# Kernel tuning notes

Measured on AMD Instinct MI355X. Metric: run time of the kernel, lower is better.

Reference implementation:

```python
import jax, jax.numpy as jnp
import numpy as np

D_MODEL, D_FF, N_EXPERTS, TOP_K = 1024, 2048, 8, 2
B, S = 2, 2048

def setup_inputs() -> dict:
    key = jax.random.key(0)
    k1, k2, k3, k4 = jax.random.split(key, 4)
    scale = 0.02
    return {
        "x": jax.random.normal(k1, (B, S, D_MODEL), dtype=jnp.float32),
        "gate_w": jax.random.normal(k2, (D_MODEL, N_EXPERTS), dtype=jnp.float32) * scale,
        "w1": jax.random.normal(k3, (N_EXPERTS, D_MODEL, D_FF), dtype=jnp.float32) * scale,
        "w2": jax.random.normal(k4, (N_EXPERTS, D_FF, D_MODEL), dtype=jnp.float32) * scale,
    }

def reference(x, gate_w, w1, w2):
    # --- Router (eval mode: no exploration noise, no dropout) ---
    router_logits = jnp.einsum('bsd,de->bse', x, gate_w)          # [B,S,E]
    top_logits, top_idx = jax.lax.top_k(router_logits, TOP_K)      # [B,S,K]
    top_w = jax.nn.softmax(top_logits, axis=-1)                    # [B,S,K]
    # topk indices are distinct per token, so per-(token,expert) combine weight
    # is the sum over k of weight_k * 1[idx_k == e] (matches torch gather/argmax logic)
    combine = jnp.sum(
        jax.nn.one_hot(top_idx, N_EXPERTS, dtype=x.dtype) * top_w[..., None],
        axis=-2)                                                   # [B,S,E]
    # --- Experts: dense-compute formulation of the gather/MLP/scatter loop ---
    h = jax.nn.silu(jnp.einsum('bsd,edf->ebsf', x, w1))            # [E,B,S,Dff]
    y = jnp.einsum('ebsf,efd->ebsd', h, w2)                        # [E,B,S,D]
    out = jnp.einsum('ebsd,bse->bsd', y, combine)                  # [B,S,D]
    return out
```

## Files before the change

kernel.cpp:

```cpp
#include <hip/hip_runtime.h>
#include <cstdint>
#include <cstddef>

#define D_MODEL 1024
#define D_FF    2048
#define N_EXP   8
#define NTOK    4096
#define NASSIGN (NTOK * 2)
#define MAXTILE 72

typedef __bf16 bf16_t;
typedef bf16_t bf16x8 __attribute__((ext_vector_type(8)));
typedef float  f32x4  __attribute__((ext_vector_type(4)));

typedef __attribute__((address_space(3))) void       lds_void;
typedef const __attribute__((address_space(1))) void gl_void;

__device__ __forceinline__ unsigned short f2b(float f) {
  union { float f; unsigned u; } v; v.f = f;
  unsigned u = v.u;
  unsigned r = (u + 0x7FFFu + ((u >> 16) & 1u)) >> 16;
  return (unsigned short)r;
}
__device__ __forceinline__ float b2f(unsigned short b) {
  union { unsigned u; float f; } v; v.u = ((unsigned)b) << 16; return v.f;
}

__device__ __forceinline__ void transpose_tile_128x64(
    const float* __restrict__ ein, unsigned short* __restrict__ eout,
    int R , int C ,
    int r0, int c0, unsigned* T, int tid)
{
  const int g = tid >> 4;
  const int m = tid & 15;

  float4 v[8];
  #pragma unroll
  for (int i = 0; i < 8; ++i)
    v[i] = *(const float4*)(ein + (size_t)(r0 + i * 16 + g) * C + c0 + m * 4);

  #pragma unroll
  for (int i = 0; i < 8; ++i) {
    int r  = i * 16 + g;
    int cx = (r >> 5) << 3;
    unsigned lo = (unsigned)f2b(v[i].x) | ((unsigned)f2b(v[i].y) << 16);
    unsigned hi = (unsigned)f2b(v[i].z) | ((unsigned)f2b(v[i].w) << 16);
    T[r * 33 + ((2 * m)     ^ cx)] = lo;
    T[r * 33 + ((2 * m + 1) ^ cx)] = hi;
  }
  __syncthreads();

  const int c    = tid >> 2;
  const int s4   = tid & 3;
  const int half = (c & 1) * 16;
  const int ccol = (c >> 1) ^ (s4 << 3);
  unsigned ow[16];
  #pragma unroll
  for (int j2 = 0; j2 < 16; ++j2) {
    int r = s4 * 32 + 2 * j2;
    unsigned lo16 = (T[r * 33 + ccol] >> half) & 0xFFFFu;
    unsigned hi16 = (T[(r + 1) * 33 + ccol] >> half) & 0xFFFFu;
    ow[j2] = lo16 | (hi16 << 16);
  }
  uint4* dst = (uint4*)(eout + (size_t)(c0 + c) * R + r0 + s4 * 32);
  dst[0] = *(uint4*)&ow[0];
  dst[1] = *(uint4*)&ow[4];
  dst[2] = *(uint4*)&ow[8];
  dst[3] = *(uint4*)&ow[12];
}

__global__ __launch_bounds__(256) void prep_k(
    const float* __restrict__ x, const float* __restrict__ gw,
    const float* __restrict__ w1, const float* __restrict__ w2,
    unsigned short* __restrict__ w1t, unsigned short* __restrict__ w2t,
    int* __restrict__ eidx, float* __restrict__ ewt)
{
  __shared__ unsigned T[128 * 33];
  const int bid = blockIdx.x;
  const int tid = threadIdx.x;

  if (bid < 2048) {
    int e = bid >> 8, rem = bid & 255;
    int by = rem >> 5, bx = rem & 31;
    transpose_tile_128x64(w1 + (size_t)e * D_MODEL * D_FF,
                          w1t + (size_t)e * D_MODEL * D_FF,
                          D_MODEL, D_FF, by * 128, bx * 64, T, tid);
    return;
  }
  if (bid < 4096) {
    int b = bid - 2048;
    int e = b >> 8, rem = b & 255;
    int by = rem >> 4, bx = rem & 15;
    transpose_tile_128x64(w2 + (size_t)e * D_MODEL * D_FF,
                          w2t + (size_t)e * D_MODEL * D_FF,
                          D_FF, D_MODEL, by * 128, bx * 64, T, tid);
    return;
  }
  const int rb = bid - 4096;
  const int wv = tid >> 6, lane = tid & 63;
  const int token = rb * 4 + wv;
  const float4* xr4 = (const float4*)(x + (size_t)token * D_MODEL);
  const float4* gw4 = (const float4*)gw;

  float acc[8] = {};
  #pragma unroll
  for (int it = 0; it < 4; ++it) {
    float4 xv = xr4[it * 64 + lane];
    int d0 = it * 256 + lane * 4;
    #pragma unroll
    for (int i = 0; i < 4; ++i) {
      int d = d0 + i;
      float4 g0 = gw4[d * 2];
      float4 g1 = gw4[d * 2 + 1];
      float xs = (i == 0) ? xv.x : (i == 1) ? xv.y : (i == 2) ? xv.z : xv.w;
      acc[0] += xs * g0.x; acc[1] += xs * g0.y;
      acc[2] += xs * g0.z; acc[3] += xs * g0.w;
      acc[4] += xs * g1.x; acc[5] += xs * g1.y;
      acc[6] += xs * g1.z; acc[7] += xs * g1.w;
    }
  }
  #pragma unroll
  for (int m = 1; m < 64; m <<= 1) {
    #pragma unroll
    for (int k = 0; k < 8; ++k) acc[k] += __shfl_xor(acc[k], m);
  }
  if (lane == 0) {
    int i1 = 0; float v1 = acc[0];
    #pragma unroll
    for (int k = 1; k < 8; ++k) if (acc[k] > v1) { v1 = acc[k]; i1 = k; }
    int i2 = -1; float v2 = -1e30f;
    #pragma unroll
    for (int k = 0; k < 8; ++k) if (k != i1 && acc[k] > v2) { v2 = acc[k]; i2 = k; }
    float t  = __expf(v2 - v1);
    float wa = 1.f / (1.f + t);
    float wb = t * wa;
    eidx[token * 2 + 0] = i1; eidx[token * 2 + 1] = i2;
    ewt [token * 2 + 0] = wa; ewt [token * 2 + 1] = wb;
  }
}

__global__ __launch_bounds__(1024) void scan_k(
    const int* __restrict__ eidx, const float* __restrict__ ewt,
    int* __restrict__ counts, int* __restrict__ offsets,
    int* __restrict__ rowtok, float* __restrict__ rowwt, int* __restrict__ rowof,
    int* __restrict__ tile_e, int* __restrict__ tile_m0, int* __restrict__ tile_n)
{
  __shared__ int wtot[16][9];
  __shared__ int woff[16][9];
  __shared__ int soff[8];
  const int t = threadIdx.x, w = t >> 6, lane = t & 63;

  int4 a = ((const int4*)eidx)[t * 2];
  int4 b = ((const int4*)eidx)[t * 2 + 1];
  int my[8] = {a.x, a.y, a.z, a.w, b.x, b.y, b.z, b.w};
  int pre[8], local[8] = {};
  #pragma unroll
  for (int i = 0; i < 8; ++i) { pre[i] = local[my[i]]; local[my[i]]++; }

  int inc[8];
  #pragma unroll
  for (int e = 0; e < 8; ++e) inc[e] = local[e];
  #pragma unroll
  for (int d = 1; d < 64; d <<= 1) {
    #pragma unroll
    for (int e = 0; e < 8; ++e) {
      int v = __shfl_up(inc[e], d);
      if (lane >= d) inc[e] += v;
    }
  }
  if (lane == 63) {
    #pragma unroll
    for (int e = 0; e < 8; ++e) wtot[w][e] = inc[e];
  }
  __syncthreads();

  if (t < 8) {
    int e = t, run = 0;
    #pragma unroll
    for (int ww = 0; ww < 16; ++ww) { woff[ww][e] = run; run += wtot[ww][e]; }
    wtot[0][e] = run;
  }
  __syncthreads();

  if (t == 0) {
    int o = 0, tt = 0;
    for (int e = 0; e < 8; ++e) {
      int c = wtot[0][e];
      counts[e] = c;
      offsets[e] = o;
      soff[e] = o;
      int nt = (c + 255) >> 8;
      for (int i = 0; i < nt; ++i) { tile_e[tt] = e; tile_m0[tt] = i * 256; ++tt; }
      o += c;
    }
    tile_n[0] = tt;
  }
  __syncthreads();

  int base_[8];
  #pragma unroll
  for (int e = 0; e < 8; ++e) base_[e] = soff[e] + woff[w][e] + inc[e] - local[e];

  float4 wa4 = ((const float4*)ewt)[t * 2];
  float4 wb4 = ((const float4*)ewt)[t * 2 + 1];
  float wv[8] = {wa4.x, wa4.y, wa4.z, wa4.w, wb4.x, wb4.y, wb4.z, wb4.w};

  #pragma unroll
  for (int i = 0; i < 8; ++i) {
    int bb = t * 8 + i, e = my[i];
    int row = base_[e] + pre[i];
    rowtok[row] = bb >> 1;
    rowwt[row]  = wv[i];
    rowof[bb]   = row;
  }
}

__global__ __launch_bounds__(256) void gather_k(
    const float* __restrict__ x, const int* __restrict__ rowtok,
    unsigned short* __restrict__ Xe)
{
  const int row = blockIdx.x;
  const int token = rowtok[row];
  const float4* xr = (const float4*)(x + (size_t)token * D_MODEL);
  ushort4* dst = (ushort4*)(Xe + (size_t)row * D_MODEL);
  float4 v = xr[threadIdx.x];
  ushort4 o;
  o.x = f2b(v.x); o.y = f2b(v.y); o.z = f2b(v.z); o.w = f2b(v.w);
  dst[threadIdx.x] = o;
}

template<int K, int N, int MODE>
__global__ __launch_bounds__(512) void moe_gemm_k(
    const unsigned short* __restrict__ A,
    const unsigned short* __restrict__ Bt,
    unsigned short* __restrict__ Hout,
    const int* __restrict__ counts, const int* __restrict__ offsets,
    const float* __restrict__ rowwt,
    const int* __restrict__ tile_e, const int* __restrict__ tile_m0,
    const int* __restrict__ tile_n)
{
  constexpr int BN    = 256;
  constexpr int RT    = 512;
  constexpr int LOADS = 8;
  constexpr int JF    = 4;
  constexpr int NT    = K / 64;
  constexpr int NTN   = N / BN;
  constexpr int WN    = 64;

  __shared__ char lds[2 * RT * 128];

  const int nwg = gridDim.x;
  const int bid = blockIdx.x;
  const int wg  = (bid & 7) * (nwg >> 3) + (bid >> 3);
  const int t_  = wg / NTN;
  if (t_ >= tile_n[0]) return;
  const int e    = tile_e[t_];
  const int m0   = tile_m0[t_];
  const int n0   = (wg % NTN) * BN;
  const int cnt  = counts[e];
  const int base = offsets[e];

  const int tid  = threadIdx.x;
  const int l    = tid & 63;
  const int w    = tid >> 6;
  const int wm   = w >> 2;
  const int wn   = w & 3;
  const int col  = l & 15, quad = l >> 4;

  const unsigned short* Aseg = A + (size_t)base * K;
  const unsigned short* Bseg = Bt + (size_t)e * ((size_t)N * K);

  const int w8 = w * 8, l3 = l >> 3;
  const int ckst = ((l & 7) ^ l3) << 3;

  auto stage_one = [&](int n, int k0s, char* bw) {
    const unsigned short* src = (n < 4)
      ? Aseg + (size_t)(m0 + n * 64 + w8 + l3) * K + (k0s + ckst)
      : Bseg + (size_t)(n0 + (n - 4) * 64 + w8 + l3) * K + (k0s + ckst);
    __builtin_amdgcn_global_load_lds((gl_void*)src,
        (lds_void*)(bw + (n * 8 + w) * 1024), 16, 0, 0);
  };

  #pragma unroll
  for (int n = 0; n < LOADS; ++n) stage_one(n, 0, lds);

  const int abyte = (wm * 128 + col) * 128;
  const int bbyte = (256 + wn * WN + col) * 128;

  f32x4 acc[8][JF] = {};

  for (int t = 0; t < NT; ++t) {
    char* bufR = lds + (t & 1) * (RT * 128);
    char* bufW = lds + ((t + 1) & 1) * (RT * 128);
    const int k0n = (t + 1) * 64;
    const bool hn = (t + 1 < NT);
    if (hn) {
      stage_one(0, k0n, bufW);
      stage_one(1, k0n, bufW);
      asm volatile("s_waitcnt vmcnt(2)" ::: "memory");
    } else {
      asm volatile("s_waitcnt vmcnt(0)" ::: "memory");
    }
    asm volatile("s_barrier" ::: "memory");

    bf16x8 bfr[JF];
    #pragma unroll
    for (int p = 0; p < 4; ++p) {
      const int ks = p >> 1, ih = p & 1;
      const int cb = ((((ks << 2) | quad) ^ (col & 7)) << 4);
      bf16x8 af[4];
      #pragma unroll
      for (int i = 0; i < 4; ++i)
        af[i] = *(const bf16x8*)(bufR + abyte + (ih * 4 + i) * 2048 + cb);
      if (ih == 0) {
        #pragma unroll
        for (int j = 0; j < JF; ++j)
          bfr[j] = *(const bf16x8*)(bufR + bbyte + j * 2048 + cb);
      }
      if (hn && p < 3) {
        stage_one(2 + 2 * p, k0n, bufW);
        stage_one(3 + 2 * p, k0n, bufW);
      }
      asm volatile("s_waitcnt lgkmcnt(0)" ::: "memory");
      __builtin_amdgcn_s_setprio(1);
      #pragma unroll
      for (int i = 0; i < 4; ++i)
        #pragma unroll
        for (int j = 0; j < JF; ++j)
          acc[ih * 4 + i][j] = __builtin_amdgcn_mfma_f32_16x16x32_bf16(
              af[i], bfr[j], acc[ih * 4 + i][j], 0, 0, 0);
      __builtin_amdgcn_s_setprio(0);
      asm volatile("s_barrier" ::: "memory");
    }
  }

  #pragma unroll
  for (int i = 0; i < 8; ++i) {
    #pragma unroll
    for (int reg = 0; reg < 4; ++reg) {
      int r = m0 + wm * 128 + i * 16 + quad * 4 + reg;
      if (r < cnt) {
        unsigned short* hrow = Hout + (size_t)(base + r) * N + (n0 + wn * WN + col);
        if (MODE == 1) {
          #pragma unroll
          for (int j = 0; j < JF; ++j) {
            float v = acc[i][j][reg];
            float s = v / (1.f + __expf(-v));
            hrow[j * 16] = f2b(s);
          }
        } else {
          float wgt = rowwt[base + r];
          #pragma unroll
          for (int j = 0; j < JF; ++j)
            hrow[j * 16] = f2b(wgt * acc[i][j][reg]);
        }
      }
    }
  }
}

__global__ __launch_bounds__(256) void combine_k(
    const unsigned short* __restrict__ Y, const int* __restrict__ rowof,
    float* __restrict__ out)
{
  const int token = blockIdx.x;
  const int r1 = rowof[token * 2];
  const int r2 = rowof[token * 2 + 1];
  const int d4 = threadIdx.x;
  ushort4 a = *(const ushort4*)(Y + (size_t)r1 * D_MODEL + d4 * 4);
  ushort4 b = *(const ushort4*)(Y + (size_t)r2 * D_MODEL + d4 * 4);
  float4 o;
  o.x = b2f(a.x) + b2f(b.x);
  o.y = b2f(a.y) + b2f(b.y);
  o.z = b2f(a.z) + b2f(b.z);
  o.w = b2f(a.w) + b2f(b.w);
  *(float4*)(out + (size_t)token * D_MODEL + d4 * 4) = o;
}

extern "C" void kernel_launch(void* const* d_in, const int* in_sizes, int n_in,
                              void* d_out, int out_size, void* d_ws, size_t ws_size,
                              hipStream_t stream) {
  const float* x  = (const float*)d_in[0];
  const float* gw = (const float*)d_in[1];
  const float* w1 = (const float*)d_in[2];
  const float* w2 = (const float*)d_in[3];
  float* out = (float*)d_out;

  char* ws = (char*)d_ws;
  size_t off = 0;
  auto alloc = [&](size_t bytes) -> char* {
    char* p = ws + off; off += (bytes + 255) & ~(size_t)255; return p;
  };
  int*   ctrl    = (int*)alloc(1024);
  int*   counts  = ctrl;
  int*   offsets = ctrl + 8;
  int*   tile_n  = ctrl + 16;
  int*   tile_e  = ctrl + 32;
  int*   tile_m0 = ctrl + 32 + MAXTILE;
  int*   eidx    = (int*)  alloc((size_t)NASSIGN * 4);
  float* ewt     = (float*)alloc((size_t)NASSIGN * 4);
  int*   rowtok  = (int*)  alloc((size_t)NASSIGN * 4);
  float* rowwt   = (float*)alloc((size_t)NASSIGN * 4);
  int*   rowof   = (int*)  alloc((size_t)NASSIGN * 4);
  unsigned short* Xe  = (unsigned short*)alloc((size_t)(NASSIGN + 256) * D_MODEL * 2);
  unsigned short* H   = (unsigned short*)alloc((size_t)(NASSIGN + 256) * D_FF * 2);
  unsigned short* Y   = (unsigned short*)alloc((size_t)(NASSIGN + 256) * D_MODEL * 2);
  unsigned short* w1t = (unsigned short*)alloc((size_t)N_EXP * D_MODEL * D_FF * 2);
  unsigned short* w2t = (unsigned short*)alloc((size_t)N_EXP * D_MODEL * D_FF * 2);

  prep_k<<<4096 + NTOK / 4, 256, 0, stream>>>(x, gw, w1, w2, w1t, w2t, eidx, ewt);
  scan_k<<<1, 1024, 0, stream>>>(eidx, ewt, counts, offsets, rowtok, rowwt, rowof,
                                 tile_e, tile_m0, tile_n);
  gather_k<<<NASSIGN, 256, 0, stream>>>(x, rowtok, Xe);

  moe_gemm_k<D_MODEL, D_FF, 1><<<320, 512, 0, stream>>>(
      Xe, w1t, H, counts, offsets, rowwt, tile_e, tile_m0, tile_n);
  moe_gemm_k<D_FF, D_MODEL, 2><<<160, 512, 0, stream>>>(
      H, w2t, Y, counts, offsets, rowwt, tile_e, tile_m0, tile_n);
  combine_k<<<NTOK, 256, 0, stream>>>(Y, rowof, out);
}
```

Baseline: 336.6 us.

## Prefetch two K-tiles ahead in expert GEMM and use direct-to-LDS loads in weight transpose

The grouped expert GEMM now preloads two K-tiles and issues the loads for tile t+2 after finishing compute on tile t. This replaces the per-subphase interleaved staging with a deeper software pipeline and fewer barriers per tile. The weight transpose kernel now loads fp32 tiles straight into LDS via global_load_lds with an XOR swizzle and converts pairs with the packed bf16 convert instruction. The change costs more LDS for the transpose tile and keeps more loads in flight, and it depends on LOADS being 8 for the vmcnt(8) wait to be correct.

```diff
diff --git a/kernel.cpp b/kernel.cpp
--- a/kernel.cpp
+++ b/kernel.cpp
@@ -25,42 +25,46 @@
 __device__ __forceinline__ float b2f(unsigned short b) {
   union { unsigned u; float f; } v; v.u = ((unsigned)b) << 16; return v.f;
 }
-
-__device__ __forceinline__ void transpose_tile_128x64(
+__device__ __forceinline__ unsigned cvt_pk_bf16(float lo, float hi) {
+  unsigned r;
+  asm("v_cvt_pk_bf16_f32 %0, %1, %2" : "=v"(r) : "v"(lo), "v"(hi));
+  return r;
+}
+
+__device__ __forceinline__ void transpose_tile_glds(
     const float* __restrict__ ein, unsigned short* __restrict__ eout,
-    int R , int C ,
-    int r0, int c0, unsigned* T, int tid)
-{
-  const int g = tid >> 4;
-  const int m = tid & 15;
-
-  float4 v[8];
-  #pragma unroll
-  for (int i = 0; i < 8; ++i)
-    v[i] = *(const float4*)(ein + (size_t)(r0 + i * 16 + g) * C + c0 + m * 4);
-
-  #pragma unroll
-  for (int i = 0; i < 8; ++i) {
-    int r  = i * 16 + g;
-    int cx = (r >> 5) << 3;
-    unsigned lo = (unsigned)f2b(v[i].x) | ((unsigned)f2b(v[i].y) << 16);
-    unsigned hi = (unsigned)f2b(v[i].z) | ((unsigned)f2b(v[i].w) << 16);
-    T[r * 33 + ((2 * m)     ^ cx)] = lo;
-    T[r * 33 + ((2 * m + 1) ^ cx)] = hi;
+    int R , int C , int r0, int c0,
+    unsigned* T , int tid)
+{
+  const int l = tid & 63;
+  const int w = tid >> 6;
+  const int p  = l & 15;
+  const int lr = l >> 4;
+
+  #pragma unroll
+  for (int n = 0; n < 8; ++n) {
+    int row = (n * 4 + w) * 4 + lr;
+    const float* src = ein + (size_t)(r0 + row) * C + c0 + (((p ^ (row & 15)) << 2));
+    __builtin_amdgcn_global_load_lds((gl_void*)src,
+        (lds_void*)((char*)T + (n * 4 + w) * 1024), 16, 0, 0);
   }
   __syncthreads();
 
-  const int c    = tid >> 2;
-  const int s4   = tid & 3;
-  const int half = (c & 1) * 16;
-  const int ccol = (c >> 1) ^ (s4 << 3);
+  const int c  = tid >> 2;
+  const int s4 = tid & 3;
+  const int pc = c >> 2, cl = c & 3;
   unsigned ow[16];
   #pragma unroll
   for (int j2 = 0; j2 < 16; ++j2) {
-    int r = s4 * 32 + 2 * j2;
-    unsigned lo16 = (T[r * 33 + ccol] >> half) & 0xFFFFu;
-    unsigned hi16 = (T[(r + 1) * 33 + ccol] >> half) & 0xFFFFu;
-    ow[j2] = lo16 | (hi16 << 16);
+    int j  = (j2 + 4 * s4) & 15;
+    int r  = s4 * 32 + 2 * j;
+    float lo, hi;
+    { unsigned u = T[r * 64 + ((pc ^ (r & 15)) << 2) + cl];
+      union { unsigned u; float f; } v; v.u = u; lo = v.f; }
+    { int r1 = r + 1;
+      unsigned u = T[r1 * 64 + ((pc ^ (r1 & 15)) << 2) + cl];
+      union { unsigned u; float f; } v; v.u = u; hi = v.f; }
+    ow[j] = cvt_pk_bf16(lo, hi);
   }
   uint4* dst = (uint4*)(eout + (size_t)(c0 + c) * R + r0 + s4 * 32);
   dst[0] = *(uint4*)&ow[0];
@@ -75,25 +79,25 @@
     unsigned short* __restrict__ w1t, unsigned short* __restrict__ w2t,
     int* __restrict__ eidx, float* __restrict__ ewt)
 {
-  __shared__ unsigned T[128 * 33];
+  __shared__ unsigned T[8192];
   const int bid = blockIdx.x;
   const int tid = threadIdx.x;
 
   if (bid < 2048) {
     int e = bid >> 8, rem = bid & 255;
     int by = rem >> 5, bx = rem & 31;
-    transpose_tile_128x64(w1 + (size_t)e * D_MODEL * D_FF,
-                          w1t + (size_t)e * D_MODEL * D_FF,
-                          D_MODEL, D_FF, by * 128, bx * 64, T, tid);
+    transpose_tile_glds(w1 + (size_t)e * D_MODEL * D_FF,
+                        w1t + (size_t)e * D_MODEL * D_FF,
+                        D_MODEL, D_FF, by * 128, bx * 64, T, tid);
     return;
   }
   if (bid < 4096) {
     int b = bid - 2048;
     int e = b >> 8, rem = b & 255;
     int by = rem >> 4, bx = rem & 15;
-    transpose_tile_128x64(w2 + (size_t)e * D_MODEL * D_FF,
-                          w2t + (size_t)e * D_MODEL * D_FF,
-                          D_FF, D_MODEL, by * 128, bx * 64, T, tid);
+    transpose_tile_glds(w2 + (size_t)e * D_MODEL * D_FF,
+                        w2t + (size_t)e * D_MODEL * D_FF,
+                        D_FF, D_MODEL, by * 128, bx * 64, T, tid);
     return;
   }
   const int rb = bid - 4096;
@@ -283,6 +287,8 @@
 
   #pragma unroll
   for (int n = 0; n < LOADS; ++n) stage_one(n, 0, lds);
+  #pragma unroll
+  for (int n = 0; n < LOADS; ++n) stage_one(n, 64, lds + RT * 128);
 
   const int abyte = (wm * 128 + col) * 128;
   const int bbyte = (256 + wn * WN + col) * 128;
@@ -291,46 +297,44 @@
 
   for (int t = 0; t < NT; ++t) {
     char* bufR = lds + (t & 1) * (RT * 128);
-    char* bufW = lds + ((t + 1) & 1) * (RT * 128);
-    const int k0n = (t + 1) * 64;
-    const bool hn = (t + 1 < NT);
-    if (hn) {
-      stage_one(0, k0n, bufW);
-      stage_one(1, k0n, bufW);
-      asm volatile("s_waitcnt vmcnt(2)" ::: "memory");
+    if (t + 1 < NT) {
+      asm volatile("s_waitcnt vmcnt(8)" ::: "memory");
     } else {
       asm volatile("s_waitcnt vmcnt(0)" ::: "memory");
     }
     asm volatile("s_barrier" ::: "memory");
 
-    bf16x8 bfr[JF];
-    #pragma unroll
-    for (int p = 0; p < 4; ++p) {
-      const int ks = p >> 1, ih = p & 1;
+    bf16x8 bfr[2][JF];
+    #pragma unroll
+    for (int ks = 0; ks < 2; ++ks) {
       const int cb = ((((ks << 2) | quad) ^ (col & 7)) << 4);
-      bf16x8 af[4];
       #pragma unroll
-      for (int i = 0; i < 4; ++i)
-        af[i] = *(const bf16x8*)(bufR + abyte + (ih * 4 + i) * 2048 + cb);
-      if (ih == 0) {
+      for (int j = 0; j < JF; ++j)
+        bfr[ks][j] = *(const bf16x8*)(bufR + bbyte + j * 2048 + cb);
+    }
+    #pragma unroll
+    for (int ks = 0; ks < 2; ++ks) {
+      const int cb = ((((ks << 2) | quad) ^ (col & 7)) << 4);
+      #pragma unroll
+      for (int ih = 0; ih < 2; ++ih) {
+        bf16x8 af[4];
         #pragma unroll
-        for (int j = 0; j < JF; ++j)
-          bfr[j] = *(const bf16x8*)(bufR + bbyte + j * 2048 + cb);
+        for (int i = 0; i < 4; ++i)
+          af[i] = *(const bf16x8*)(bufR + abyte + (ih * 4 + i) * 2048 + cb);
+        __builtin_amdgcn_s_setprio(1);
+        #pragma unroll
+        for (int i = 0; i < 4; ++i)
+          #pragma unroll
+          for (int j = 0; j < JF; ++j)
+            acc[ih * 4 + i][j] = __builtin_amdgcn_mfma_f32_16x16x32_bf16(
+                af[i], bfr[ks][j], acc[ih * 4 + i][j], 0, 0, 0);
+        __builtin_amdgcn_s_setprio(0);
       }
-      if (hn && p < 3) {
-        stage_one(2 + 2 * p, k0n, bufW);
-        stage_one(3 + 2 * p, k0n, bufW);
-      }
-      asm volatile("s_waitcnt lgkmcnt(0)" ::: "memory");
-      __builtin_amdgcn_s_setprio(1);
+    }
+    asm volatile("s_barrier" ::: "memory");
+    if (t + 2 < NT) {
       #pragma unroll
-      for (int i = 0; i < 4; ++i)
-        #pragma unroll
-        for (int j = 0; j < JF; ++j)
-          acc[ih * 4 + i][j] = __builtin_amdgcn_mfma_f32_16x16x32_bf16(
-              af[i], bfr[j], acc[ih * 4 + i][j], 0, 0, 0);
-      __builtin_amdgcn_s_setprio(0);
-      asm volatile("s_barrier" ::: "memory");
+      for (int n = 0; n < LOADS; ++n) stage_one(n, (t + 2) * 64, bufR);
     }
   }
 
```

After: 380.2 us. +13.0%, slower.

## Prefetch two K-tiles ahead and drop per-phase barriers in expert GEMM

Applied to the files above, without the earlier changes.

The GEMM mainloop now fills both LDS buffers up front. Each iteration waits only for the older tile (vmcnt(8)) and issues loads for tile t+2 into the buffer it just consumed, after one end-of-iteration barrier. This replaces the loads previously interleaved across four phases, each with its own barrier. B fragments for both k-substeps are read once per tile, and the explicit lgkmcnt waits are left to the compiler. The aim is deeper memory latency hiding and fewer barriers, at the cost of more registers for the doubled B fragments and a correctness dependence on the hardcoded vmcnt matching LOADS.

```diff
diff --git a/kernel.cpp b/kernel.cpp
--- a/kernel.cpp
+++ b/kernel.cpp
@@ -283,6 +283,8 @@
 
   #pragma unroll
   for (int n = 0; n < LOADS; ++n) stage_one(n, 0, lds);
+  #pragma unroll
+  for (int n = 0; n < LOADS; ++n) stage_one(n, 64, lds + RT * 128);
 
   const int abyte = (wm * 128 + col) * 128;
   const int bbyte = (256 + wn * WN + col) * 128;
@@ -291,46 +293,44 @@
 
   for (int t = 0; t < NT; ++t) {
     char* bufR = lds + (t & 1) * (RT * 128);
-    char* bufW = lds + ((t + 1) & 1) * (RT * 128);
-    const int k0n = (t + 1) * 64;
-    const bool hn = (t + 1 < NT);
-    if (hn) {
-      stage_one(0, k0n, bufW);
-      stage_one(1, k0n, bufW);
-      asm volatile("s_waitcnt vmcnt(2)" ::: "memory");
+    if (t + 1 < NT) {
+      asm volatile("s_waitcnt vmcnt(8)" ::: "memory");
     } else {
       asm volatile("s_waitcnt vmcnt(0)" ::: "memory");
     }
     asm volatile("s_barrier" ::: "memory");
 
-    bf16x8 bfr[JF];
-    #pragma unroll
-    for (int p = 0; p < 4; ++p) {
-      const int ks = p >> 1, ih = p & 1;
+    bf16x8 bfr[2][JF];
+    #pragma unroll
+    for (int ks = 0; ks < 2; ++ks) {
       const int cb = ((((ks << 2) | quad) ^ (col & 7)) << 4);
-      bf16x8 af[4];
       #pragma unroll
-      for (int i = 0; i < 4; ++i)
-        af[i] = *(const bf16x8*)(bufR + abyte + (ih * 4 + i) * 2048 + cb);
-      if (ih == 0) {
+      for (int j = 0; j < JF; ++j)
+        bfr[ks][j] = *(const bf16x8*)(bufR + bbyte + j * 2048 + cb);
+    }
+    #pragma unroll
+    for (int ks = 0; ks < 2; ++ks) {
+      const int cb = ((((ks << 2) | quad) ^ (col & 7)) << 4);
+      #pragma unroll
+      for (int ih = 0; ih < 2; ++ih) {
+        bf16x8 af[4];
         #pragma unroll
-        for (int j = 0; j < JF; ++j)
-          bfr[j] = *(const bf16x8*)(bufR + bbyte + j * 2048 + cb);
+        for (int i = 0; i < 4; ++i)
+          af[i] = *(const bf16x8*)(bufR + abyte + (ih * 4 + i) * 2048 + cb);
+        __builtin_amdgcn_s_setprio(1);
+        #pragma unroll
+        for (int i = 0; i < 4; ++i)
+          #pragma unroll
+          for (int j = 0; j < JF; ++j)
+            acc[ih * 4 + i][j] = __builtin_amdgcn_mfma_f32_16x16x32_bf16(
+                af[i], bfr[ks][j], acc[ih * 4 + i][j], 0, 0, 0);
+        __builtin_amdgcn_s_setprio(0);
       }
-      if (hn && p < 3) {
-        stage_one(2 + 2 * p, k0n, bufW);
-        stage_one(3 + 2 * p, k0n, bufW);
-      }
-      asm volatile("s_waitcnt lgkmcnt(0)" ::: "memory");
-      __builtin_amdgcn_s_setprio(1);
+    }
+    asm volatile("s_barrier" ::: "memory");
+    if (t + 2 < NT) {
       #pragma unroll
-      for (int i = 0; i < 4; ++i)
-        #pragma unroll
-        for (int j = 0; j < JF; ++j)
-          acc[ih * 4 + i][j] = __builtin_amdgcn_mfma_f32_16x16x32_bf16(
-              af[i], bfr[j], acc[ih * 4 + i][j], 0, 0, 0);
-      __builtin_amdgcn_s_setprio(0);
-      asm volatile("s_barrier" ::: "memory");
+      for (int n = 0; n < LOADS; ++n) stage_one(n, (t + 2) * 64, bufR);
     }
   }
 
```

Measured after the change: 357.3 us. 1.06x slower.
